# Kernel optimization log

Measured on AMD Instinct MI355X. Metric: run time of the kernel, lower is better.

The kernel has to match this reference:

```python
import jax, jax.numpy as jnp
import numpy as np

B, C, T, N = 8, 128, 64, 256
D_STATE, D_CONV, EXPAND = 4, 3, 1
D_INNER = EXPAND * C
DT_RANK = (C + 15) // 16  # 8


def setup_inputs() -> dict:
    key = jax.random.key(0)
    ks = jax.random.split(key, 8)
    s = lambda k, shape, sc=0.02: jax.random.normal(k, shape, jnp.float32) * sc
    return {
        "x": jax.random.normal(ks[0], (B, C, T, N), jnp.float32),
        "ln_gamma": jnp.ones((C,), jnp.float32),
        "ln_beta": jnp.zeros((C,), jnp.float32),
        "in_proj_w": s(ks[1], (2 * D_INNER, C)),
        "conv_w": s(ks[2], (D_CONV, 1, D_INNER), 0.1),
        "conv_b": jnp.zeros((D_INNER,), jnp.float32),
        "x_proj_w": s(ks[3], (DT_RANK + 2 * D_STATE, D_INNER)),
        "dt_proj_w": s(ks[4], (D_INNER, DT_RANK), 0.1),
        "dt_proj_b": s(ks[5], (D_INNER,), 0.1),
        "A_log": jnp.log(jnp.broadcast_to(jnp.arange(1, D_STATE + 1, dtype=jnp.float32), (D_INNER, D_STATE))),
        "D": jnp.ones((D_INNER,), jnp.float32),
        "out_proj_w": s(ks[6], (C, D_INNER)),
    }


def _mamba(x, in_proj_w, conv_w, conv_b, x_proj_w, dt_proj_w, dt_proj_b, A_log, D, out_proj_w):
    # x: (BN, T, C) -- selective-scan Mamba block, single (forward) direction
    xz = x @ in_proj_w.T                                   # (BN, T, 2*D_INNER)
    xc, z = jnp.split(xz, 2, axis=-1)
    # causal depthwise conv along time
    xp = jnp.pad(xc, ((0, 0), (D_CONV - 1, 0), (0, 0)))
    xc = jax.lax.conv_general_dilated(
        xp, conv_w, (1,), 'VALID',
        dimension_numbers=('NWC', 'WIO', 'NWC'),
        feature_group_count=D_INNER) + conv_b
    xc = jax.nn.silu(xc)
    x_dbl = xc @ x_proj_w.T                                # (BN, T, DT_RANK + 2*D_STATE)
    dt, Bs, Cs = jnp.split(x_dbl, [DT_RANK, DT_RANK + D_STATE], axis=-1)
    dt = jax.nn.softplus(dt @ dt_proj_w.T + dt_proj_b)     # (BN, T, D_INNER)
    A = -jnp.exp(A_log)                                    # (D_INNER, D_STATE)
    dA = jnp.exp(dt[..., None] * A)                        # (BN, T, D_INNER, D_STATE)
    dBx = dt[..., None] * Bs[:, :, None, :] * xc[..., None]

    def step(h, inps):
        dA_t, dBx_t, C_t = inps
        h = h * dA_t + dBx_t                               # (BN, D_INNER, D_STATE)
        y = jnp.einsum('bdn,bn->bd', h, C_t)
        return h, y

    h0 = jnp.zeros((xc.shape[0], D_INNER, D_STATE), xc.dtype)
    _, ys = jax.lax.scan(step, h0, (dA.transpose(1, 0, 2, 3),
                                    dBx.transpose(1, 0, 2, 3),
                                    Cs.transpose(1, 0, 2)))
    y = ys.transpose(1, 0, 2) + xc * D                     # (BN, T, D_INNER)
    y = y * jax.nn.silu(z)                                 # gate (if_divide_out=False)
    return y @ out_proj_w.T


def reference(x, ln_gamma, ln_beta, in_proj_w, conv_w, conv_b, x_proj_w,
              dt_proj_w, dt_proj_b, A_log, D, out_proj_w):
    # (B, C, T, N) -> (B, T, N, C)
    h = x.transpose(0, 2, 3, 1)
    mu = h.mean(-1, keepdims=True)
    var = h.var(-1, keepdims=True)
    h = (h - mu) / jnp.sqrt(var + 1e-5) * ln_gamma + ln_beta
    h = h.astype(jnp.float32)  # fp32 cast (autocast disabled around mamba)
    bb, tt, nn, cc = h.shape
    # temporal mode: each (batch, node) pair is an independent time sequence
    hs = h.transpose(0, 2, 1, 3).reshape(bb * nn, tt, cc)
    y = _mamba(hs, in_proj_w, conv_w, conv_b, x_proj_w, dt_proj_w, dt_proj_b,
               A_log, D, out_proj_w)
    y = y.reshape(bb, nn, tt, cc).transpose(0, 2, 1, 3)    # (B, T, N, C)
    return y.transpose(0, 3, 1, 2)                         # (B, C, T, N)
```

## Files before the change

kernel.cpp:

```cpp
#include <hip/hip_runtime.h>
#include <math.h>

#define B_   8
#define C_   128
#define T_   64
#define N_   256
#define NSEQ 8

typedef __attribute__((ext_vector_type(8))) short bf16x8;
typedef __attribute__((ext_vector_type(4))) float f32x4;
typedef unsigned short ushort_t;

#define LOG2E 1.4426950408889634f
#define LN2   0.6931471805599453f

#define R0   0
#define R1   8448
#define RXD  17152
#define RXT  18432
#define LDSW 27136

#define SELH 0x05040100u
#define SELL 0x07060302u

__device__ __forceinline__ unsigned bfhi(float x) {
  unsigned u = __float_as_uint(x);
  return (u + 0x7FFF + ((u >> 16) & 1)) >> 16;
}
__device__ __forceinline__ unsigned packsplit(float x) {
  unsigned hi = bfhi(x);
  float rem = x - __uint_as_float(hi << 16);
  unsigned lo = bfhi(rem);
  return (hi & 0xFFFFu) | (lo << 16);
}
__device__ __forceinline__ float fsilu(float v) {
  return v * __builtin_amdgcn_rcpf(1.0f + __builtin_amdgcn_exp2f(-LOG2E * v));
}
__device__ __forceinline__ float qsum4(float v) {
  int x = __builtin_amdgcn_update_dpp(0, __float_as_int(v), 0xB1, 0xF, 0xF, true);
  v += __int_as_float(x);
  x = __builtin_amdgcn_update_dpp(0, __float_as_int(v), 0x4E, 0xF, 0xF, true);
  v += __int_as_float(x);
  return v;
}
union BU { uint4 q; bf16x8 v; unsigned u[4]; };

__global__ __launch_bounds__(512) void k_wsplit(const float* __restrict__ Win,
                                                const float* __restrict__ Wout,
                                                const float* __restrict__ Wx,
                                                ushort_t* __restrict__ wsi,
                                                ushort_t* __restrict__ wso,
                                                ushort_t* __restrict__ wsx) {
  int idx = blockIdx.x * 512 + threadIdx.x;
  const float* src;
  ushort_t* dst;
  if (idx < 1024) {
    int row = idx >> 2, kc = idx & 3;
    src = Win + row * 128 + kc * 32;
    dst = wsi + (row * 4 + kc) * 64;
  } else if (idx < 1536) {
    int k = idx - 1024;
    int row = k >> 2, kc = k & 3;
    src = Wout + row * 128 + kc * 32;
    dst = wso + (row * 4 + kc) * 64;
  } else if (idx < 1600) {
    int k = idx - 1536;
    int row = k >> 2, kc = k & 3;
    src = Wx + row * 128 + kc * 32;
    dst = wsx + (row * 4 + kc) * 64;
  } else {
    return;
  }
  for (int g = 0; g < 4; ++g) {
    unsigned hw[4], lw[4];
#pragma unroll
    for (int e2 = 0; e2 < 4; ++e2) {
      float x0 = src[g * 8 + 2 * e2], x1 = src[g * 8 + 2 * e2 + 1];
      unsigned p0 = packsplit(x0), p1 = packsplit(x1);
      hw[e2] = (p0 & 0xFFFFu) | (p1 << 16);
      lw[e2] = (p0 >> 16) | (p1 & 0xFFFF0000u);
    }
    *(uint4*)(dst + (g * 2 + 0) * 8) = make_uint4(hw[0], hw[1], hw[2], hw[3]);
    *(uint4*)(dst + (g * 2 + 1) * 8) = make_uint4(lw[0], lw[1], lw[2], lw[3]);
  }
}

__global__ __launch_bounds__(256) void k_ln(const float* __restrict__ x,
                                            const float* __restrict__ gam,
                                            const float* __restrict__ bet,
                                            float* __restrict__ hout) {
  __shared__ float tile[128 * 36];
  __shared__ float ps[8 * 32], pq[8 * 32], mean_s[32], rstd_s[32];
  int bx = blockIdx.x;
  int nt = bx & 7, t = (bx >> 3) & 63, b = bx >> 9;
  int n0 = nt * 32;
  int tid = threadIdx.x;
  const float4* x4 = (const float4*)x;
  for (int it = 0; it < 4; ++it) {
    int idx4 = it * 256 + tid;
    int c = idx4 >> 3, nn4 = idx4 & 7;
    float4 v = x4[((b * C_ + c) * T_ + t) * (N_ / 4) + (n0 >> 2) + nn4];
    *(float4*)&tile[c * 36 + nn4 * 4] = v;
  }
  __syncthreads();
  {
    int nn = tid & 31, cg = tid >> 5;
    float s = 0.f, q = 0.f;
    for (int i = 0; i < 16; ++i) {
      float v = tile[(cg * 16 + i) * 36 + nn];
      s += v; q += v * v;
    }
    ps[cg * 32 + nn] = s; pq[cg * 32 + nn] = q;
  }
  __syncthreads();
  if (tid < 32) {
    float ss = 0.f, qq = 0.f;
    for (int g2 = 0; g2 < 8; ++g2) { ss += ps[g2 * 32 + tid]; qq += pq[g2 * 32 + tid]; }
    float mu = ss * (1.f / 128.f);
    float var = qq * (1.f / 128.f) - mu * mu;
    mean_s[tid] = mu;
    rstd_s[tid] = rsqrtf(var + 1e-5f);
  }
  __syncthreads();
  {
    int c = tid & 127, half = tid >> 7;
    float gm = gam[c], bb = bet[c];
    for (int it = 0; it < 16; ++it) {
      int n = it * 2 + half;
      float v = (tile[c * 36 + n] - mean_s[n]) * rstd_s[n] * gm + bb;
      hout[((b * N_ + n0 + n) * (long)T_ + t) * C_ + c] = v;
    }
  }
}

__global__ __launch_bounds__(512, 2) void k_mamba(
    float* ws,
    const ushort_t* __restrict__ wsi,
    const ushort_t* __restrict__ wso,
    const ushort_t* __restrict__ wsx,
    const float* __restrict__ convw,
    const float* __restrict__ convb,
    const float* __restrict__ Wdt,
    const float* __restrict__ bdt,
    const float* __restrict__ Alog,
    const float* __restrict__ Dp)
{
  extern __shared__ float L[];
  unsigned* Li = (unsigned*)L;
  int tid = threadIdx.x;
  int lane = tid & 63;
  int w = tid >> 6;
  int r16 = lane & 15, g = lane >> 4;
  const uint4* wsi4 = (const uint4*)wsi;
  const uint4* wso4 = (const uint4*)wso;
  const uint4* wsx4 = (const uint4*)wsx;

  uint4 wih[2][4], wil[2][4], woh[4], wol[4];
#pragma unroll
  for (int ci = 0; ci < 2; ++ci)
#pragma unroll
    for (int kc = 0; kc < 4; ++kc) {
      int cb = ((w * 32 + ci * 16 + r16) * 4 + kc) * 8 + g * 2;
      wih[ci][kc] = wsi4[cb];
      wil[ci][kc] = wsi4[cb + 1];
    }
#pragma unroll
  for (int kc = 0; kc < 4; ++kc) {
    int cb = ((w * 16 + r16) * 4 + kc) * 8 + g * 2;
    woh[kc] = wso4[cb];
    wol[kc] = wso4[cb + 1];
  }
  int dc = tid & 127, tq = tid >> 7;
  float cw0 = convw[dc], cw1 = convw[128 + dc], cw2 = convw[256 + dc];
  float cbv = convb[dc];
  int ds = tid >> 2, ss = tid & 3;
  float wA = Wdt[ds * 8 + 2 * ss], wB = Wdt[ds * 8 + 2 * ss + 1];
  float bd = bdt[ds];
  float As2 = -expf(Alog[ds * 4 + ss]) * LOG2E;
  float Dd = Dp[ds];

  for (int iseq = 0; iseq < NSEQ; ++iseq) {
    float* hseq = ws + ((long)blockIdx.x * NSEQ + iseq) * (T_ * C_);

    {
      const float4* h4 = (const float4*)hseq;
      int ts = tid >> 3, kg = tid & 7;
      int sw = (ts & 7) << 2;
#pragma unroll
      for (int q = 0; q < 4; ++q) {
        float4 v = h4[ts * 32 + kg * 4 + q];
        uint4 pw = make_uint4(packsplit(v.x), packsplit(v.y), packsplit(v.z), packsplit(v.w));
        *(uint4*)&Li[R0 + ts * 132 + ((kg * 16 + q * 4) ^ sw)] = pw;
      }
    }
    __syncthreads();

    f32x4 acc[4][2];
#pragma unroll
    for (int rt = 0; rt < 4; ++rt)
#pragma unroll
      for (int ci = 0; ci < 2; ++ci) acc[rt][ci] = (f32x4){0.f, 0.f, 0.f, 0.f};
#pragma unroll
    for (int kc = 0; kc < 4; ++kc) {
#pragma unroll
      for (int rt = 0; rt < 4; ++rt) {
        int row = rt * 16 + r16;
        int sw = (row & 7) << 2;
        int base = R0 + row * 132 + kc * 32;
        uint4 wa = *(const uint4*)&Li[base + ((g * 8) ^ sw)];
        uint4 wb = *(const uint4*)&Li[base + ((g * 8 + 4) ^ sw)];
        BU ah, al;
        ah.u[0] = __builtin_amdgcn_perm(wa.y, wa.x, SELH);
        ah.u[1] = __builtin_amdgcn_perm(wa.w, wa.z, SELH);
        ah.u[2] = __builtin_amdgcn_perm(wb.y, wb.x, SELH);
        ah.u[3] = __builtin_amdgcn_perm(wb.w, wb.z, SELH);
        al.u[0] = __builtin_amdgcn_perm(wa.y, wa.x, SELL);
        al.u[1] = __builtin_amdgcn_perm(wa.w, wa.z, SELL);
        al.u[2] = __builtin_amdgcn_perm(wb.y, wb.x, SELL);
        al.u[3] = __builtin_amdgcn_perm(wb.w, wb.z, SELL);
#pragma unroll
        for (int ci = 0; ci < 2; ++ci) {
          BU bh, bl;
          bh.q = wih[ci][kc];
          bl.q = wil[ci][kc];
          acc[rt][ci] = __builtin_amdgcn_mfma_f32_16x16x32_bf16(al.v, bh.v, acc[rt][ci], 0, 0, 0);
          acc[rt][ci] = __builtin_amdgcn_mfma_f32_16x16x32_bf16(ah.v, bl.v, acc[rt][ci], 0, 0, 0);
          acc[rt][ci] = __builtin_amdgcn_mfma_f32_16x16x32_bf16(ah.v, bh.v, acc[rt][ci], 0, 0, 0);
        }
      }
    }
    __syncthreads();

    {
      int dl0 = (w & 3) * 32;
      if (w < 4) {
#pragma unroll
        for (int rt = 0; rt < 4; ++rt)
#pragma unroll
          for (int ci = 0; ci < 2; ++ci)
#pragma unroll
            for (int r = 0; r < 4; ++r)
              L[R0 + (rt * 16 + g * 4 + r) * 132 + dl0 + ci * 16 + r16] = acc[rt][ci][r];
      } else {
#pragma unroll
        for (int rt = 0; rt < 4; ++rt)
#pragma unroll
          for (int ci = 0; ci < 2; ++ci)
#pragma unroll
            for (int r = 0; r < 4; ++r)
              L[R1 + (dl0 + ci * 16 + r16) * 68 + rt * 16 + g * 4 + r] = fsilu(acc[rt][ci][r]);
      }
    }
    __syncthreads();

    {
      int t0 = tq * 16;
      float xin[18];
#pragma unroll
      for (int ii = 0; ii < 18; ++ii) {
        int t = t0 - 2 + ii;
        xin[ii] = (t < 0) ? 0.f : L[R0 + t * 132 + dc];
      }
      __syncthreads();
      float sv[16];
#pragma unroll
      for (int ii = 0; ii < 16; ++ii) {
        float v = fmaf(cw2, xin[ii + 2], fmaf(cw1, xin[ii + 1], fmaf(cw0, xin[ii], cbv)));
        sv[ii] = fsilu(v);
      }
#pragma unroll
      for (int ii = 0; ii < 16; ++ii) {
        int t = t0 + ii;
        Li[R0 + t * 132 + (dc ^ ((t & 7) << 2))] = packsplit(sv[ii]);
      }
#pragma unroll
      for (int qq = 0; qq < 4; ++qq)
        *(float4*)&L[RXT + dc * 68 + t0 + qq * 4] =
            make_float4(sv[qq * 4], sv[qq * 4 + 1], sv[qq * 4 + 2], sv[qq * 4 + 3]);
    }
    __syncthreads();

    if (w < 4) {
      f32x4 o = (f32x4){0.f, 0.f, 0.f, 0.f};
#pragma unroll
      for (int kc = 0; kc < 4; ++kc) {
        int cb = (r16 * 4 + kc) * 8 + g * 2;
        BU bh, bl;
        bh.q = wsx4[cb];
        bl.q = wsx4[cb + 1];
        int row = w * 16 + r16;
        int sw = (row & 7) << 2;
        int base = R0 + row * 132 + kc * 32;
        uint4 wa = *(const uint4*)&Li[base + ((g * 8) ^ sw)];
        uint4 wb = *(const uint4*)&Li[base + ((g * 8 + 4) ^ sw)];
        BU ah, al;
        ah.u[0] = __builtin_amdgcn_perm(wa.y, wa.x, SELH);
        ah.u[1] = __builtin_amdgcn_perm(wa.w, wa.z, SELH);
        ah.u[2] = __builtin_amdgcn_perm(wb.y, wb.x, SELH);
        ah.u[3] = __builtin_amdgcn_perm(wb.w, wb.z, SELH);
        al.u[0] = __builtin_amdgcn_perm(wa.y, wa.x, SELL);
        al.u[1] = __builtin_amdgcn_perm(wa.w, wa.z, SELL);
        al.u[2] = __builtin_amdgcn_perm(wb.y, wb.x, SELL);
        al.u[3] = __builtin_amdgcn_perm(wb.w, wb.z, SELL);
        o = __builtin_amdgcn_mfma_f32_16x16x32_bf16(al.v, bh.v, o, 0, 0, 0);
        o = __builtin_amdgcn_mfma_f32_16x16x32_bf16(ah.v, bl.v, o, 0, 0, 0);
        o = __builtin_amdgcn_mfma_f32_16x16x32_bf16(ah.v, bh.v, o, 0, 0, 0);
      }
      int p = (r16 < 8) ? ((r16 >> 1) * 4 + (r16 & 1))
                        : (r16 < 12 ? (r16 - 8) * 4 + 2 : (r16 - 12) * 4 + 3);
#pragma unroll
      for (int q = 0; q < 4; ++q)
        L[RXD + (w * 16 + g * 4 + q) * 20 + p] = o[q];
    }
    __syncthreads();

    {
      float h = 0.f;
#pragma unroll
      for (int tb = 0; tb < 16; ++tb) {
        float4 xq = *(const float4*)&L[RXT + ds * 68 + tb * 4];
        float4 zq = *(const float4*)&L[R1 + ds * 68 + tb * 4];
        float xcl[4] = {xq.x, xq.y, xq.z, xq.w};
        float zl[4] = {zq.x, zq.y, zq.z, zq.w};
#pragma unroll
        for (int si = 0; si < 4; ++si) {
          int t = tb * 4 + si;
          float4 xd = *(const float4*)&L[RXD + t * 20 + ss * 4];
          float dtv = qsum4(fmaf(xd.x, wA, xd.y * wB)) + bd;
          float e = __builtin_amdgcn_exp2f(dtv * LOG2E);
          float sp = LN2 * __builtin_amdgcn_logf(1.0f + e);
          dtv = (dtv > 20.f) ? dtv : sp;
          float xcv = xcl[si];
          float dA = __builtin_amdgcn_exp2f(dtv * As2);
          h = fmaf(h, dA, dtv * xcv * xd.z);
          float y = qsum4(h * xd.w);
          if (si == ss) {
            y = fmaf(xcv, Dd, y);
            y *= zl[si];
            Li[R0 + t * 132 + (ds ^ ((t & 7) << 2))] = packsplit(y);
          }
        }
      }
    }
    __syncthreads();

    {
      f32x4 o[4];
#pragma unroll
      for (int rt = 0; rt < 4; ++rt) o[rt] = (f32x4){0.f, 0.f, 0.f, 0.f};
#pragma unroll
      for (int kc = 0; kc < 4; ++kc) {
        BU bh, bl;
        bh.q = woh[kc];
        bl.q = wol[kc];
#pragma unroll
        for (int rt = 0; rt < 4; ++rt) {
          int row = rt * 16 + r16;
          int sw = (row & 7) << 2;
          int base = R0 + row * 132 + kc * 32;
          uint4 wa = *(const uint4*)&Li[base + ((g * 8) ^ sw)];
          uint4 wb = *(const uint4*)&Li[base + ((g * 8 + 4) ^ sw)];
          BU ah, al;
          ah.u[0] = __builtin_amdgcn_perm(wa.y, wa.x, SELH);
          ah.u[1] = __builtin_amdgcn_perm(wa.w, wa.z, SELH);
          ah.u[2] = __builtin_amdgcn_perm(wb.y, wb.x, SELH);
          ah.u[3] = __builtin_amdgcn_perm(wb.w, wb.z, SELH);
          al.u[0] = __builtin_amdgcn_perm(wa.y, wa.x, SELL);
          al.u[1] = __builtin_amdgcn_perm(wa.w, wa.z, SELL);
          al.u[2] = __builtin_amdgcn_perm(wb.y, wb.x, SELL);
          al.u[3] = __builtin_amdgcn_perm(wb.w, wb.z, SELL);
          o[rt] = __builtin_amdgcn_mfma_f32_16x16x32_bf16(al.v, bh.v, o[rt], 0, 0, 0);
          o[rt] = __builtin_amdgcn_mfma_f32_16x16x32_bf16(ah.v, bl.v, o[rt], 0, 0, 0);
          o[rt] = __builtin_amdgcn_mfma_f32_16x16x32_bf16(ah.v, bh.v, o[rt], 0, 0, 0);
        }
      }
#pragma unroll
      for (int rt = 0; rt < 4; ++rt)
#pragma unroll
        for (int r = 0; r < 4; ++r)
          hseq[(rt * 16 + g * 4 + r) * C_ + w * 16 + r16] = o[rt][r];
    }
    __syncthreads();
  }
}

__global__ __launch_bounds__(256) void k_out_tr(const float* __restrict__ ws_y,
                                                float* __restrict__ out) {
  __shared__ float tile[32 * 132];
  int bx = blockIdx.x;
  int nt = bx & 7, t = (bx >> 3) & 63, b = bx >> 9;
  int n0 = nt * 32;
  int tid = threadIdx.x;
  const float4* y4 = (const float4*)ws_y;
  for (int it = 0; it < 4; ++it) {
    int idx4 = it * 256 + tid;
    int nn = idx4 >> 5, c4 = idx4 & 31;
    float4 v = y4[((b * N_ + n0 + nn) * (long)T_ + t) * (C_ / 4) + c4];
    *(float4*)&tile[nn * 132 + c4 * 4] = v;
  }
  __syncthreads();
  int nn = tid & 31, cg = tid >> 5;
  for (int i = 0; i < 16; ++i) {
    int c = cg * 16 + i;
    out[((b * C_ + c) * (long)T_ + t) * N_ + n0 + nn] = tile[nn * 132 + c];
  }
}

extern "C" void kernel_launch(void* const* d_in, const int* in_sizes, int n_in,
                              void* d_out, int out_size, void* d_ws, size_t ws_size,
                              hipStream_t stream) {
  const float* x    = (const float*)d_in[0];
  const float* gam  = (const float*)d_in[1];
  const float* bet  = (const float*)d_in[2];
  const float* Win  = (const float*)d_in[3];
  const float* cw   = (const float*)d_in[4];
  const float* cb   = (const float*)d_in[5];
  const float* Wx   = (const float*)d_in[6];
  const float* Wdt  = (const float*)d_in[7];
  const float* bdt  = (const float*)d_in[8];
  const float* Alog = (const float*)d_in[9];
  const float* Dp   = (const float*)d_in[10];
  const float* Wout = (const float*)d_in[11];
  float* out = (float*)d_out;
  float* ws  = (float*)d_ws;

  const size_t HBYTES = 67108864ull;
  const size_t WBYTES = 131072ull + 65536ull + 8192ull;
  char* wtail;
  if (ws_size >= HBYTES + WBYTES) wtail = (char*)d_ws + HBYTES;
  else                            wtail = (char*)d_out;
  ushort_t* wsi = (ushort_t*)wtail;
  ushort_t* wso = (ushort_t*)(wtail + 131072);
  ushort_t* wsx = (ushort_t*)(wtail + 131072 + 65536);

  (void)hipFuncSetAttribute((const void*)k_mamba,
                            hipFuncAttributeMaxDynamicSharedMemorySize,
                            LDSW * 4);

  k_wsplit<<<4, 512, 0, stream>>>(Win, Wout, Wx, wsi, wso, wsx);
  k_ln<<<4096, 256, 0, stream>>>(x, gam, bet, ws);
  k_mamba<<<2048 / NSEQ, 512, LDSW * 4, stream>>>(ws, wsi, wso, wsx, cw, cb,
                                                  Wdt, bdt, Alog, Dp);
  k_out_tr<<<4096, 256, 0, stream>>>(ws, out);
}
```

Baseline: 218.5 us.

## Shrink LDS footprint, rotate swizzle, raise occupancy to four blocks per CU

```diff
diff --git a/kernel.cpp b/kernel.cpp
--- a/kernel.cpp
+++ b/kernel.cpp
@@ -5,7 +5,7 @@
 #define C_   128
 #define T_   64
 #define N_   256
-#define NSEQ 8
+#define NSEQ 4
 
 typedef __attribute__((ext_vector_type(8))) short bf16x8;
 typedef __attribute__((ext_vector_type(4))) float f32x4;
@@ -16,9 +16,8 @@
 
 #define R0   0
 #define R1   8448
-#define RXD  17152
-#define RXT  18432
-#define LDSW 27136
+#define RXD  17024
+#define LDSW 18304
 
 #define SELH 0x05040100u
 #define SELL 0x07060302u
@@ -32,6 +31,9 @@
   float rem = x - __uint_as_float(hi << 16);
   unsigned lo = bfhi(rem);
   return (hi & 0xFFFFu) | (lo << 16);
+}
+__device__ __forceinline__ float unpacksplit(unsigned u) {
+  return __uint_as_float(u << 16) + __uint_as_float(u & 0xFFFF0000u);
 }
 __device__ __forceinline__ float fsilu(float v) {
   return v * __builtin_amdgcn_rcpf(1.0f + __builtin_amdgcn_exp2f(-LOG2E * v));
@@ -42,6 +44,10 @@
   x = __builtin_amdgcn_update_dpp(0, __float_as_int(v), 0x4E, 0xF, 0xF, true);
   v += __int_as_float(x);
   return v;
+}
+__device__ __forceinline__ int sigq(int qk) { return (qk >> 1) | ((qk & 1) << 2); }
+__device__ __forceinline__ int kpos(int k, int s) {
+  return (k & ~31) + ((((sigq((k >> 2) & 7)) + s) & 7) << 2) + (k & 3);
 }
 union BU { uint4 q; bf16x8 v; unsigned u[4]; };
 
@@ -133,7 +139,7 @@
   }
 }
 
-__global__ __launch_bounds__(512, 2) void k_mamba(
+__global__ __launch_bounds__(512, 4) void k_mamba(
     float* ws,
     const ushort_t* __restrict__ wsi,
     const ushort_t* __restrict__ wso,
@@ -170,7 +176,7 @@
     woh[kc] = wso4[cb];
     wol[kc] = wso4[cb + 1];
   }
-  int dc = tid & 127, tq = tid >> 7;
+  int dc = tid & 127;
   float cw0 = convw[dc], cw1 = convw[128 + dc], cw2 = convw[256 + dc];
   float cbv = convb[dc];
   int ds = tid >> 2, ss = tid & 3;
@@ -178,6 +184,8 @@
   float bd = bdt[ds];
   float As2 = -expf(Alog[ds * 4 + ss]) * LOG2E;
   float Dd = Dp[ds];
+  int kc_d = (ds & ~31) + (ds & 3);
+  int qs_d = sigq((ds >> 2) & 7);
 
   for (int iseq = 0; iseq < NSEQ; ++iseq) {
     float* hseq = ws + ((long)blockIdx.x * NSEQ + iseq) * (T_ * C_);
@@ -185,12 +193,13 @@
     {
       const float4* h4 = (const float4*)hseq;
       int ts = tid >> 3, kg = tid & 7;
-      int sw = (ts & 7) << 2;
+      int s = ts & 7;
+      int slot = (sigq(kg) + s) & 7;
 #pragma unroll
       for (int q = 0; q < 4; ++q) {
-        float4 v = h4[ts * 32 + kg * 4 + q];
+        float4 v = h4[ts * 32 + kg + 8 * q];
         uint4 pw = make_uint4(packsplit(v.x), packsplit(v.y), packsplit(v.z), packsplit(v.w));
-        *(uint4*)&Li[R0 + ts * 132 + ((kg * 16 + q * 4) ^ sw)] = pw;
+        *(uint4*)&Li[R0 + ts * 132 + q * 32 + slot * 4] = pw;
       }
     }
     __syncthreads();
@@ -200,32 +209,34 @@
     for (int rt = 0; rt < 4; ++rt)
 #pragma unroll
       for (int ci = 0; ci < 2; ++ci) acc[rt][ci] = (f32x4){0.f, 0.f, 0.f, 0.f};
-#pragma unroll
-    for (int kc = 0; kc < 4; ++kc) {
-#pragma unroll
-      for (int rt = 0; rt < 4; ++rt) {
-        int row = rt * 16 + r16;
-        int sw = (row & 7) << 2;
-        int base = R0 + row * 132 + kc * 32;
-        uint4 wa = *(const uint4*)&Li[base + ((g * 8) ^ sw)];
-        uint4 wb = *(const uint4*)&Li[base + ((g * 8 + 4) ^ sw)];
-        BU ah, al;
-        ah.u[0] = __builtin_amdgcn_perm(wa.y, wa.x, SELH);
-        ah.u[1] = __builtin_amdgcn_perm(wa.w, wa.z, SELH);
-        ah.u[2] = __builtin_amdgcn_perm(wb.y, wb.x, SELH);
-        ah.u[3] = __builtin_amdgcn_perm(wb.w, wb.z, SELH);
-        al.u[0] = __builtin_amdgcn_perm(wa.y, wa.x, SELL);
-        al.u[1] = __builtin_amdgcn_perm(wa.w, wa.z, SELL);
-        al.u[2] = __builtin_amdgcn_perm(wb.y, wb.x, SELL);
-        al.u[3] = __builtin_amdgcn_perm(wb.w, wb.z, SELL);
-#pragma unroll
-        for (int ci = 0; ci < 2; ++ci) {
-          BU bh, bl;
-          bh.q = wih[ci][kc];
-          bl.q = wil[ci][kc];
-          acc[rt][ci] = __builtin_amdgcn_mfma_f32_16x16x32_bf16(al.v, bh.v, acc[rt][ci], 0, 0, 0);
-          acc[rt][ci] = __builtin_amdgcn_mfma_f32_16x16x32_bf16(ah.v, bl.v, acc[rt][ci], 0, 0, 0);
-          acc[rt][ci] = __builtin_amdgcn_mfma_f32_16x16x32_bf16(ah.v, bh.v, acc[rt][ci], 0, 0, 0);
+    {
+      int s = r16 & 7;
+      int slotA = (g + s) & 7, slotB = (g + 4 + s) & 7;
+#pragma unroll
+      for (int kc = 0; kc < 4; ++kc) {
+#pragma unroll
+        for (int rt = 0; rt < 4; ++rt) {
+          int base = R0 + (rt * 16 + r16) * 132 + kc * 32;
+          uint4 wa = *(const uint4*)&Li[base + slotA * 4];
+          uint4 wb = *(const uint4*)&Li[base + slotB * 4];
+          BU ah, al;
+          ah.u[0] = __builtin_amdgcn_perm(wa.y, wa.x, SELH);
+          ah.u[1] = __builtin_amdgcn_perm(wa.w, wa.z, SELH);
+          ah.u[2] = __builtin_amdgcn_perm(wb.y, wb.x, SELH);
+          ah.u[3] = __builtin_amdgcn_perm(wb.w, wb.z, SELH);
+          al.u[0] = __builtin_amdgcn_perm(wa.y, wa.x, SELL);
+          al.u[1] = __builtin_amdgcn_perm(wa.w, wa.z, SELL);
+          al.u[2] = __builtin_amdgcn_perm(wb.y, wb.x, SELL);
+          al.u[3] = __builtin_amdgcn_perm(wb.w, wb.z, SELL);
+#pragma unroll
+          for (int ci = 0; ci < 2; ++ci) {
+            BU bh, bl;
+            bh.q = wih[ci][kc];
+            bl.q = wil[ci][kc];
+            acc[rt][ci] = __builtin_amdgcn_mfma_f32_16x16x32_bf16(al.v, bh.v, acc[rt][ci], 0, 0, 0);
+            acc[rt][ci] = __builtin_amdgcn_mfma_f32_16x16x32_bf16(ah.v, bl.v, acc[rt][ci], 0, 0, 0);
+            acc[rt][ci] = __builtin_amdgcn_mfma_f32_16x16x32_bf16(ah.v, bh.v, acc[rt][ci], 0, 0, 0);
+          }
         }
       }
     }
@@ -248,12 +259,13 @@
           for (int ci = 0; ci < 2; ++ci)
 #pragma unroll
             for (int r = 0; r < 4; ++r)
-              L[R1 + (dl0 + ci * 16 + r16) * 68 + rt * 16 + g * 4 + r] = fsilu(acc[rt][ci][r]);
-      }
-    }
-    __syncthreads();
-
-    {
+              L[R1 + (dl0 + ci * 16 + r16) * 67 + rt * 16 + g * 4 + r] = fsilu(acc[rt][ci][r]);
+      }
+    }
+    __syncthreads();
+
+    {
+      int tq = tid >> 7;
       int t0 = tq * 16;
       float xin[18];
 #pragma unroll
@@ -262,25 +274,18 @@
         xin[ii] = (t < 0) ? 0.f : L[R0 + t * 132 + dc];
       }
       __syncthreads();
-      float sv[16];
-#pragma unroll
-      for (int ii = 0; ii < 16; ++ii) {
-        float v = fmaf(cw2, xin[ii + 2], fmaf(cw1, xin[ii + 1], fmaf(cw0, xin[ii], cbv)));
-        sv[ii] = fsilu(v);
-      }
 #pragma unroll
       for (int ii = 0; ii < 16; ++ii) {
         int t = t0 + ii;
-        Li[R0 + t * 132 + (dc ^ ((t & 7) << 2))] = packsplit(sv[ii]);
-      }
-#pragma unroll
-      for (int qq = 0; qq < 4; ++qq)
-        *(float4*)&L[RXT + dc * 68 + t0 + qq * 4] =
-            make_float4(sv[qq * 4], sv[qq * 4 + 1], sv[qq * 4 + 2], sv[qq * 4 + 3]);
+        float v = fmaf(cw2, xin[ii + 2], fmaf(cw1, xin[ii + 1], fmaf(cw0, xin[ii], cbv)));
+        Li[R0 + t * 132 + kpos(dc, t & 7)] = packsplit(fsilu(v));
+      }
     }
     __syncthreads();
 
     if (w < 4) {
+      int s = r16 & 7;
+      int slotA = (g + s) & 7, slotB = (g + 4 + s) & 7;
       f32x4 o = (f32x4){0.f, 0.f, 0.f, 0.f};
 #pragma unroll
       for (int kc = 0; kc < 4; ++kc) {
@@ -288,11 +293,9 @@
         BU bh, bl;
         bh.q = wsx4[cb];
         bl.q = wsx4[cb + 1];
-        int row = w * 16 + r16;
-        int sw = (row & 7) << 2;
-        int base = R0 + row * 132 + kc * 32;
-        uint4 wa = *(const uint4*)&Li[base + ((g * 8) ^ sw)];
-        uint4 wb = *(const uint4*)&Li[base + ((g * 8 + 4) ^ sw)];
+        int base = R0 + (w * 16 + r16) * 132 + kc * 32;
+        uint4 wa = *(const uint4*)&Li[base + slotA * 4];
+        uint4 wb = *(const uint4*)&Li[base + slotB * 4];
         BU ah, al;
         ah.u[0] = __builtin_amdgcn_perm(wa.y, wa.x, SELH);
         ah.u[1] = __builtin_amdgcn_perm(wa.w, wa.z, SELH);
@@ -316,35 +319,30 @@
 
     {
       float h = 0.f;
-#pragma unroll
-      for (int tb = 0; tb < 16; ++tb) {
-        float4 xq = *(const float4*)&L[RXT + ds * 68 + tb * 4];
-        float4 zq = *(const float4*)&L[R1 + ds * 68 + tb * 4];
-        float xcl[4] = {xq.x, xq.y, xq.z, xq.w};
-        float zl[4] = {zq.x, zq.y, zq.z, zq.w};
-#pragma unroll
-        for (int si = 0; si < 4; ++si) {
-          int t = tb * 4 + si;
-          float4 xd = *(const float4*)&L[RXD + t * 20 + ss * 4];
-          float dtv = qsum4(fmaf(xd.x, wA, xd.y * wB)) + bd;
-          float e = __builtin_amdgcn_exp2f(dtv * LOG2E);
-          float sp = LN2 * __builtin_amdgcn_logf(1.0f + e);
-          dtv = (dtv > 20.f) ? dtv : sp;
-          float xcv = xcl[si];
-          float dA = __builtin_amdgcn_exp2f(dtv * As2);
-          h = fmaf(h, dA, dtv * xcv * xd.z);
-          float y = qsum4(h * xd.w);
-          if (si == ss) {
-            y = fmaf(xcv, Dd, y);
-            y *= zl[si];
-            Li[R0 + t * 132 + (ds ^ ((t & 7) << 2))] = packsplit(y);
-          }
+#pragma unroll 8
+      for (int t = 0; t < 64; ++t) {
+        float4 xd = *(const float4*)&L[RXD + t * 20 + ss * 4];
+        float dtv = qsum4(fmaf(xd.x, wA, xd.y * wB)) + bd;
+        float e = __builtin_amdgcn_exp2f(dtv * LOG2E);
+        float sp = LN2 * __builtin_amdgcn_logf(1.0f + e);
+        dtv = (dtv > 20.f) ? dtv : sp;
+        int xoff = R0 + t * 132 + kc_d + (((qs_d + (t & 7)) & 7) << 2);
+        float xcv = unpacksplit(Li[xoff]);
+        float dA = __builtin_amdgcn_exp2f(dtv * As2);
+        h = fmaf(h, dA, dtv * xcv * xd.z);
+        float y = qsum4(h * xd.w);
+        if ((t & 3) == ss) {
+          y = fmaf(xcv, Dd, y);
+          y *= L[R1 + ds * 67 + t];
+          Li[xoff] = packsplit(y);
         }
       }
     }
     __syncthreads();
 
     {
+      int s = r16 & 7;
+      int slotA = (g + s) & 7, slotB = (g + 4 + s) & 7;
       f32x4 o[4];
 #pragma unroll
       for (int rt = 0; rt < 4; ++rt) o[rt] = (f32x4){0.f, 0.f, 0.f, 0.f};
@@ -355,11 +353,9 @@
         bl.q = wol[kc];
 #pragma unroll
         for (int rt = 0; rt < 4; ++rt) {
-          int row = rt * 16 + r16;
-          int sw = (row & 7) << 2;
-          int base = R0 + row * 132 + kc * 32;
-          uint4 wa = *(const uint4*)&Li[base + ((g * 8) ^ sw)];
-          uint4 wb = *(const uint4*)&Li[base + ((g * 8 + 4) ^ sw)];
+          int base = R0 + (rt * 16 + r16) * 132 + kc * 32;
+          uint4 wa = *(const uint4*)&Li[base + slotA * 4];
+          uint4 wb = *(const uint4*)&Li[base + slotB * 4];
           BU ah, al;
           ah.u[0] = __builtin_amdgcn_perm(wa.y, wa.x, SELH);
           ah.u[1] = __builtin_amdgcn_perm(wa.w, wa.z, SELH);
```

Result: slower. 238.0 us (+8.9%).
